# Kernel tuning notes

Hardware: AMD Instinct MI355X
Metric: run time of the kernel (lower is better)

The kernel has to match this reference:

```python
import math
import jax, jax.numpy as jnp
import numpy as np

B, S, E, H = 4, 2048, 1024, 16
HD = E // H  # 64


def setup_inputs() -> dict:
    key = jax.random.key(0)
    ks = jax.random.split(key, 7)
    scale = 1.0 / math.sqrt(E)
    return {
        "x": jax.random.normal(ks[0], (B, S, E), dtype=jnp.float32),
        "Wq": jax.random.normal(ks[1], (H, HD, E), dtype=jnp.float32) * scale,
        "bq": jax.random.normal(ks[2], (H, HD), dtype=jnp.float32) * 0.01,
        "Wk": jax.random.normal(ks[3], (H, HD, E), dtype=jnp.float32) * scale,
        "bk": jax.random.normal(ks[4], (H, HD), dtype=jnp.float32) * 0.01,
        "Wv": jax.random.normal(ks[5], (H, HD, E), dtype=jnp.float32) * scale,
        "bv": jax.random.normal(ks[6], (H, HD), dtype=jnp.float32) * 0.01,
    }


def reference(x, Wq, bq, Wk, bk, Wv, bv):
    b, s, e = x.shape
    h, hd, _ = Wq.shape
    inv_scale = 1.0 / math.sqrt(hd)
    # per-head linear projections (torch Linear: x @ W^T + b), batched over heads
    q = jnp.einsum("bse,hde->bshd", x, Wq) + bq  # [B,S,H,HD]
    k = jnp.einsum("bse,hde->bshd", x, Wk) + bk
    v = jnp.einsum("bse,hde->bshd", x, Wv) + bv
    # causal mask: -inf above diagonal (added before scaling, as in source;
    # -inf * inv_scale is still -inf so math is identical)
    mask = jnp.triu(jnp.full((s, s), -jnp.inf, dtype=x.dtype), k=1)
    scores = (jnp.einsum("bqhd,bkhd->bhqk", q, k) + mask) * inv_scale  # [B,H,S,S]
    attn = jax.nn.softmax(scores, axis=-1)
    out = jnp.einsum("bhqk,bkhd->bqhd", attn, v)  # [B,S,H,HD]
    # concat over heads in head order == reshape with head-major last dims
    return out.reshape(b, s, h * hd)
```

## Files before the change

kernel.cpp:

```cpp
#include <hip/hip_runtime.h>


typedef __bf16 bf16x8 __attribute__((ext_vector_type(8)));
typedef __bf16 bf16x4 __attribute__((ext_vector_type(4)));
typedef float f32x4 __attribute__((ext_vector_type(4)));
typedef unsigned short us8 __attribute__((ext_vector_type(8)));
typedef unsigned short us4 __attribute__((ext_vector_type(4)));

#define Bb 4
#define Ss 2048
#define Ee 1024
#define Hh 16
#define HD 64

#if __has_builtin(__builtin_amdgcn_exp2f)
#define EXP2(x) __builtin_amdgcn_exp2f(x)
#else
#define EXP2(x) exp2f(x)
#endif

__device__ __forceinline__ unsigned short f2bf(float f) {
  union { float f; unsigned u; } v; v.f = f;
  unsigned u = v.u;
  u += 0x7fffu + ((u >> 16) & 1u);
  return (unsigned short)(u >> 16);
}

__device__ __forceinline__ void gl_lds16(const void* g, void* l) {
  __builtin_amdgcn_global_load_lds((const __attribute__((address_space(1))) void*)g,
                                   (__attribute__((address_space(3))) void*)l, 16, 0, 0);
}

#define DSR(d, a, o) asm volatile("ds_read_b128 %0, %1 offset:" #o : "=v"(d) : "v"(a))

__global__ __launch_bounds__(256) void cvt_all(const float* __restrict__ x,
                                               const float* __restrict__ wq,
                                               const float* __restrict__ wk,
                                               const float* __restrict__ wv,
                                               unsigned short* __restrict__ xb,
                                               unsigned short* __restrict__ wb) {
  int i = blockIdx.x * 256 + threadIdx.x;
  const float* src; unsigned short* dst; int idx;
  if (i < 2097152)      { src = x;  dst = xb;                idx = i; }
  else if (i < 2359296) { src = wq; dst = wb;                idx = i - 2097152; }
  else if (i < 2621440) { src = wk; dst = wb + 1048576;      idx = i - 2359296; }
  else                  { src = wv; dst = wb + 2 * 1048576;  idx = i - 2621440; }
  float4 f = ((const float4*)src)[idx];
  us4 o = { f2bf(f.x), f2bf(f.y), f2bf(f.z), f2bf(f.w) };
  ((us4*)dst)[idx] = o;
}

__global__ __launch_bounds__(256, 2) void qkv_gemm(const unsigned short* __restrict__ xb,
                                                   const unsigned short* __restrict__ wb_all,
                                                   const float* __restrict__ bq,
                                                   const float* __restrict__ bk,
                                                   const float* __restrict__ bv,
                                                   unsigned short* __restrict__ qkv) {
  const int z = blockIdx.z;
  const unsigned short* wb = wb_all + (size_t)z * (Ee * Ee);
  const float* bias = (z == 0) ? bq : (z == 1) ? bk : bv;
  unsigned short* outb = qkv + (size_t)z * (Bb * Ss * Ee);
  const float osc = (z == 0) ? 0.180336880f : 1.0f;

  __shared__ unsigned short SMEM[32768];

  const int t = threadIdx.x;
  const int wave = t >> 6, lane = t & 63, quad = lane >> 4, ln = lane & 15;
  const int wr = wave >> 1, wc = wave & 1;
  const int m0 = blockIdx.x * 128, n0 = blockIdx.y * 128;

  const int r32 = t >> 3;
  const int cs = ((t & 7) ^ (r32 & 7)) * 8;
  const int t8 = t * 8;
  const unsigned short* gA0 = xb + (size_t)(m0 + r32) * Ee + cs;
  const unsigned short* gA1 = gA0 + 64 * Ee;
  const unsigned short* gB0 = wb + (size_t)(n0 + r32) * Ee + cs;
  const unsigned short* gB1 = gB0 + 64 * Ee;

  const int swz0 = ((0 * 4 + quad) ^ (ln & 7)) * 16;
  const int swz1 = ((1 * 4 + quad) ^ (ln & 7)) * 16;
  int aA0 = (wr * 32 + ln) * 128 + swz0;
  int aA1 = (wr * 32 + ln) * 128 + swz1;
  int bA0 = 16384 + (wc * 32 + ln) * 128 + swz0;
  int bA1 = 16384 + (wc * 32 + ln) * 128 + swz1;

  f32x4 acc[2][2][2][2] = {};
  bf16x8 af[2][2], bf0[2][2], bf1[2][2];

  gl_lds16(gA0,           &SMEM[t8]);
  gl_lds16(gA0 + 32 * Ee, &SMEM[t8 + 2048]);
  gl_lds16(gB0,           &SMEM[8192 + t8]);
  gl_lds16(gB0 + 32 * Ee, &SMEM[8192 + t8 + 2048]);
  gl_lds16(gB1,           &SMEM[12288 + t8]);
  gl_lds16(gB1 + 32 * Ee, &SMEM[12288 + t8 + 2048]);
  gl_lds16(gA1,           &SMEM[4096 + t8]);
  gl_lds16(gA1 + 32 * Ee, &SMEM[4096 + t8 + 2048]);

#pragma unroll 1
  for (int kt = 0; kt < 15; ++kt) {
    const int sbuf = ((kt & 1) << 14) ^ 16384;
    const int co = (kt + 1) * 64;

    asm volatile("s_waitcnt vmcnt(4)" ::: "memory");
    asm volatile("s_barrier" ::: "memory");
    DSR(af[0][0], aA0, 0);    DSR(af[1][0], aA0, 2048);
    DSR(af[0][1], aA1, 0);    DSR(af[1][1], aA1, 2048);
    DSR(bf0[0][0], bA0, 0);   DSR(bf0[1][0], bA0, 2048);
    DSR(bf0[0][1], bA1, 0);   DSR(bf0[1][1], bA1, 2048);
    gl_lds16(gA0 + co,           &SMEM[sbuf + t8]);
    gl_lds16(gA0 + co + 32 * Ee, &SMEM[sbuf + t8 + 2048]);
    asm volatile("s_barrier" ::: "memory");
    asm volatile("s_waitcnt lgkmcnt(0)" ::: "memory");
    __builtin_amdgcn_sched_barrier(0);
    __builtin_amdgcn_s_setprio(1);
#pragma unroll
    for (int kk = 0; kk < 2; ++kk)
#pragma unroll
      for (int i = 0; i < 2; ++i)
#pragma unroll
        for (int j = 0; j < 2; ++j)
          acc[0][0][i][j] = __builtin_amdgcn_mfma_f32_16x16x32_bf16(af[i][kk], bf0[j][kk], acc[0][0][i][j], 0, 0, 0);
    __builtin_amdgcn_s_setprio(0);
    __builtin_amdgcn_sched_barrier(0);

    asm volatile("s_waitcnt vmcnt(4)" ::: "memory");
    asm volatile("s_barrier" ::: "memory");
    DSR(bf1[0][0], bA0, 8192); DSR(bf1[1][0], bA0, 10240);
    DSR(bf1[0][1], bA1, 8192); DSR(bf1[1][1], bA1, 10240);
    gl_lds16(gB0 + co,           &SMEM[sbuf + 8192 + t8]);
    gl_lds16(gB0 + co + 32 * Ee, &SMEM[sbuf + 8192 + t8 + 2048]);
    asm volatile("s_barrier" ::: "memory");
    asm volatile("s_waitcnt lgkmcnt(0)" ::: "memory");
    __builtin_amdgcn_sched_barrier(0);
    __builtin_amdgcn_s_setprio(1);
#pragma unroll
    for (int kk = 0; kk < 2; ++kk)
#pragma unroll
      for (int i = 0; i < 2; ++i)
#pragma unroll
        for (int j = 0; j < 2; ++j)
          acc[0][1][i][j] = __builtin_amdgcn_mfma_f32_16x16x32_bf16(af[i][kk], bf1[j][kk], acc[0][1][i][j], 0, 0, 0);
    __builtin_amdgcn_s_setprio(0);
    __builtin_amdgcn_sched_barrier(0);

    asm volatile("s_waitcnt vmcnt(4)" ::: "memory");
    asm volatile("s_barrier" ::: "memory");
    DSR(af[0][0], aA0, 8192); DSR(af[1][0], aA0, 10240);
    DSR(af[0][1], aA1, 8192); DSR(af[1][1], aA1, 10240);
    gl_lds16(gB1 + co,           &SMEM[sbuf + 12288 + t8]);
    gl_lds16(gB1 + co + 32 * Ee, &SMEM[sbuf + 12288 + t8 + 2048]);
    asm volatile("s_barrier" ::: "memory");
    asm volatile("s_waitcnt lgkmcnt(0)" ::: "memory");
    __builtin_amdgcn_sched_barrier(0);
    __builtin_amdgcn_s_setprio(1);
#pragma unroll
    for (int kk = 0; kk < 2; ++kk)
#pragma unroll
      for (int i = 0; i < 2; ++i)
#pragma unroll
        for (int j = 0; j < 2; ++j)
          acc[1][0][i][j] = __builtin_amdgcn_mfma_f32_16x16x32_bf16(af[i][kk], bf0[j][kk], acc[1][0][i][j], 0, 0, 0);
    __builtin_amdgcn_s_setprio(0);
    __builtin_amdgcn_sched_barrier(0);

    asm volatile("s_barrier" ::: "memory");
    gl_lds16(gA1 + co,           &SMEM[sbuf + 4096 + t8]);
    gl_lds16(gA1 + co + 32 * Ee, &SMEM[sbuf + 4096 + t8 + 2048]);
    asm volatile("s_barrier" ::: "memory");
    __builtin_amdgcn_sched_barrier(0);
    __builtin_amdgcn_s_setprio(1);
#pragma unroll
    for (int kk = 0; kk < 2; ++kk)
#pragma unroll
      for (int i = 0; i < 2; ++i)
#pragma unroll
        for (int j = 0; j < 2; ++j)
          acc[1][1][i][j] = __builtin_amdgcn_mfma_f32_16x16x32_bf16(af[i][kk], bf1[j][kk], acc[1][1][i][j], 0, 0, 0);
    __builtin_amdgcn_s_setprio(0);
    __builtin_amdgcn_sched_barrier(0);

    aA0 ^= 32768; aA1 ^= 32768; bA0 ^= 32768; bA1 ^= 32768;
  }

  {
    asm volatile("s_waitcnt vmcnt(0)" ::: "memory");
    asm volatile("s_barrier" ::: "memory");
    DSR(af[0][0], aA0, 0);    DSR(af[1][0], aA0, 2048);
    DSR(af[0][1], aA1, 0);    DSR(af[1][1], aA1, 2048);
    DSR(bf0[0][0], bA0, 0);   DSR(bf0[1][0], bA0, 2048);
    DSR(bf0[0][1], bA1, 0);   DSR(bf0[1][1], bA1, 2048);
    DSR(bf1[0][0], bA0, 8192); DSR(bf1[1][0], bA0, 10240);
    DSR(bf1[0][1], bA1, 8192); DSR(bf1[1][1], bA1, 10240);
    asm volatile("s_waitcnt lgkmcnt(0)" ::: "memory");
    __builtin_amdgcn_sched_barrier(0);
#pragma unroll
    for (int kk = 0; kk < 2; ++kk)
#pragma unroll
      for (int i = 0; i < 2; ++i)
#pragma unroll
        for (int j = 0; j < 2; ++j) {
          acc[0][0][i][j] = __builtin_amdgcn_mfma_f32_16x16x32_bf16(af[i][kk], bf0[j][kk], acc[0][0][i][j], 0, 0, 0);
          acc[0][1][i][j] = __builtin_amdgcn_mfma_f32_16x16x32_bf16(af[i][kk], bf1[j][kk], acc[0][1][i][j], 0, 0, 0);
        }
    __builtin_amdgcn_sched_barrier(0);
    DSR(af[0][0], aA0, 8192); DSR(af[1][0], aA0, 10240);
    DSR(af[0][1], aA1, 8192); DSR(af[1][1], aA1, 10240);
    asm volatile("s_waitcnt lgkmcnt(0)" ::: "memory");
    __builtin_amdgcn_sched_barrier(0);
#pragma unroll
    for (int kk = 0; kk < 2; ++kk)
#pragma unroll
      for (int i = 0; i < 2; ++i)
#pragma unroll
        for (int j = 0; j < 2; ++j) {
          acc[1][0][i][j] = __builtin_amdgcn_mfma_f32_16x16x32_bf16(af[i][kk], bf0[j][kk], acc[1][0][i][j], 0, 0, 0);
          acc[1][1][i][j] = __builtin_amdgcn_mfma_f32_16x16x32_bf16(af[i][kk], bf1[j][kk], acc[1][1][i][j], 0, 0, 0);
        }
    __builtin_amdgcn_sched_barrier(0);
  }

  float biasj[2][2];
#pragma unroll
  for (int qb = 0; qb < 2; ++qb)
#pragma unroll
    for (int j = 0; j < 2; ++j)
      biasj[qb][j] = bias[n0 + qb * 64 + wc * 32 + j * 16 + ln];

  if (z != 2) {
#pragma unroll
    for (int qa = 0; qa < 2; ++qa)
#pragma unroll
      for (int qb = 0; qb < 2; ++qb)
#pragma unroll
        for (int i = 0; i < 2; ++i)
#pragma unroll
          for (int j = 0; j < 2; ++j)
#pragma unroll
            for (int r = 0; r < 4; ++r) {
              int m = m0 + qa * 64 + wr * 32 + i * 16 + quad * 4 + r;
              int n = n0 + qb * 64 + wc * 32 + j * 16 + ln;
              int b_ = m >> 11, s = m & 2047;
              int h = n >> 6, d = n & 63;
              outb[(((size_t)b_ * Hh + h) * Ss + s) * HD + d] =
                  f2bf((acc[qa][qb][i][j][r] + biasj[qb][j]) * osc);
            }
  } else {
    __syncthreads();
#pragma unroll
    for (int qa = 0; qa < 2; ++qa)
#pragma unroll
      for (int qb = 0; qb < 2; ++qb)
#pragma unroll
        for (int i = 0; i < 2; ++i)
#pragma unroll
          for (int j = 0; j < 2; ++j)
#pragma unroll
            for (int r = 0; r < 4; ++r) {
              int nc = qb * 64 + wc * 32 + j * 16 + ln;
              int mr = qa * 64 + wr * 32 + i * 16 + quad * 4 + r;
              SMEM[nc * 136 + mr] = f2bf(acc[qa][qb][i][j][r] + biasj[qb][j]);
            }
    __syncthreads();
    int nr = t >> 1, mh = t & 1;
    int n = n0 + nr, h = n >> 6, d = n & 63;
    int b_ = m0 >> 11;
    int s0 = (m0 & 2047) + mh * 64;
#pragma unroll
    for (int q = 0; q < 8; ++q) {
      us8 vdat = *(const us8*)&SMEM[nr * 136 + mh * 64 + q * 8];
      *(us8*)&outb[(((size_t)b_ * Hh + h) * HD + d) * Ss + s0 + q * 8] = vdat;
    }
  }
}

__global__ __launch_bounds__(256, 2) void flash_attn(const unsigned short* __restrict__ qkv,
                                                     float* __restrict__ out) {
  const int id = blockIdx.x;
  const int bh = id & 63;
  const int p = id >> 6;
  const int b_ = bh >> 4, h = bh & 15;

  const unsigned short* qb  = qkv + (size_t)bh * (Ss * HD);
  const unsigned short* kb  = qkv + (size_t)(64 + bh) * (Ss * HD);
  const unsigned short* vtb = qkv + (size_t)(128 + bh) * (Ss * HD);

  __shared__ __bf16 Ks[8192];
  __shared__ __bf16 Vt[8192];
  __shared__ __bf16 Ps[4][16][72];

  const int t = threadIdx.x;
  const int wave = t >> 6, lane = t & 63, quad = lane >> 4, ln = lane & 15;

  const int rk = t >> 3;
  const int ck = ((t & 7) ^ (rk & 7)) * 8;
  const int rv = t >> 4;
  const int cv = ((t & 15) ^ (rv & 7)) * 8;
  const int t8 = t * 8;

  const int qts[2] = { 15 - p, p };
  const int KTB = qts[0] + 1;

  bf16x8 qf[2][2][2];
#pragma unroll
  for (int qt = 0; qt < 2; ++qt)
#pragma unroll
    for (int u = 0; u < 2; ++u)
#pragma unroll
      for (int ks = 0; ks < 2; ++ks)
        qf[qt][u][ks] = *(const bf16x8*)(qb + (size_t)(qts[qt] * 128 + u * 64 + wave * 16 + ln) * HD +
                                         ks * 32 + quad * 8);

  bf16x8 onef;
#pragma unroll
  for (int j = 0; j < 8; ++j) onef[j] = (__bf16)1.0f;

  f32x4 o[2][2][4] = {};
  f32x4 l4[2][2] = {};

#pragma unroll 1
  for (int kt = 0; kt < KTB; ++kt) {
    const unsigned short* kbt = kb + (size_t)kt * (128 * HD);
    const unsigned short* vbt = vtb + kt * 128;
    __syncthreads();
    gl_lds16(kbt + rk * HD + ck,        &Ks[t8]);
    gl_lds16(kbt + (rk + 32) * HD + ck, &Ks[t8 + 2048]);
    gl_lds16(kbt + (rk + 64) * HD + ck, &Ks[t8 + 4096]);
    gl_lds16(kbt + (rk + 96) * HD + ck, &Ks[t8 + 6144]);
    gl_lds16(vbt + rv * Ss + cv,        &Vt[t8]);
    gl_lds16(vbt + (rv + 16) * Ss + cv, &Vt[t8 + 2048]);
    gl_lds16(vbt + (rv + 32) * Ss + cv, &Vt[t8 + 4096]);
    gl_lds16(vbt + (rv + 48) * Ss + cv, &Vt[t8 + 6144]);
    __syncthreads();

#pragma unroll
    for (int h2 = 0; h2 < 2; ++h2) {
      const int kb64 = kt * 2 + h2;
#pragma unroll
      for (int qt = 0; qt < 2; ++qt) {
        const int qtp = qts[qt];
#pragma unroll
        for (int u = 0; u < 2; ++u) {
          const int su = 2 * qtp + u;
          if (kb64 > su) continue;
          const int qrow = qtp * 128 + u * 64 + wave * 16 + ln;

          f32x4 s_acc[4] = {};
#pragma unroll
          for (int g = 0; g < 4; ++g)
#pragma unroll
            for (int ks = 0; ks < 2; ++ks) {
              bf16x8 kf = *(const bf16x8*)&Ks[(h2 * 64 + g * 16 + ln) * 64 +
                                              (((ks * 4 + quad) ^ (ln & 7)) * 8)];
              s_acc[g] = __builtin_amdgcn_mfma_f32_16x16x32_bf16(kf, qf[qt][u][ks], s_acc[g], 0, 0, 0);
            }

          if (kb64 == su) {
            const int k0 = kb64 * 64;
#pragma unroll
            for (int g = 0; g < 4; ++g)
#pragma unroll
              for (int r = 0; r < 4; ++r) {
                int kcol = k0 + g * 16 + quad * 4 + r;
                if (kcol > qrow) s_acc[g][r] = -__builtin_inff();
              }
          }

#pragma unroll
          for (int g = 0; g < 4; ++g) {
            bf16x4 pk = { (__bf16)EXP2(s_acc[g][0]), (__bf16)EXP2(s_acc[g][1]),
                          (__bf16)EXP2(s_acc[g][2]), (__bf16)EXP2(s_acc[g][3]) };
            *(bf16x4*)&Ps[wave][ln][g * 16 + quad * 4] = pk;
          }
          bf16x8 pf[2];
#pragma unroll
          for (int ks = 0; ks < 2; ++ks)
            pf[ks] = *(const bf16x8*)&Ps[wave][ln][ks * 32 + quad * 8];

          l4[qt][u] = __builtin_amdgcn_mfma_f32_16x16x32_bf16(pf[0], onef, l4[qt][u], 0, 0, 0);
          l4[qt][u] = __builtin_amdgcn_mfma_f32_16x16x32_bf16(pf[1], onef, l4[qt][u], 0, 0, 0);

#pragma unroll
          for (int g = 0; g < 4; ++g)
#pragma unroll
            for (int ks = 0; ks < 2; ++ks) {
              bf16x8 vf = *(const bf16x8*)&Vt[(g * 16 + ln) * 128 +
                                              (((h2 * 8 + ks * 4 + quad) ^ (ln & 7)) * 8)];
              o[qt][u][g] = __builtin_amdgcn_mfma_f32_16x16x32_bf16(pf[ks], vf, o[qt][u][g], 0, 0, 0);
            }
        }
      }
    }
  }

#pragma unroll
  for (int qt = 0; qt < 2; ++qt)
#pragma unroll
    for (int u = 0; u < 2; ++u) {
      float linv[4];
#pragma unroll
      for (int r = 0; r < 4; ++r) linv[r] = 1.0f / l4[qt][u][r];
#pragma unroll
      for (int g = 0; g < 4; ++g)
#pragma unroll
        for (int r = 0; r < 4; ++r) {
          int orow = qts[qt] * 128 + u * 64 + wave * 16 + quad * 4 + r;
          out[((size_t)b_ * Ss + orow) * Ee + h * HD + g * 16 + ln] = o[qt][u][g][r] * linv[r];
        }
    }
}

extern "C" void kernel_launch(void* const* d_in, const int* in_sizes, int n_in,
                              void* d_out, int out_size, void* d_ws, size_t ws_size,
                              hipStream_t stream) {
  const float* x  = (const float*)d_in[0];
  const float* Wq = (const float*)d_in[1];
  const float* bq = (const float*)d_in[2];
  const float* Wk = (const float*)d_in[3];
  const float* bk = (const float*)d_in[4];
  const float* Wv = (const float*)d_in[5];
  const float* bv = (const float*)d_in[6];
  float* out = (float*)d_out;

  unsigned short* ws  = (unsigned short*)d_ws;
  unsigned short* xb  = ws;
  unsigned short* wb  = ws + 8388608;
  unsigned short* qkv = ws + 8388608 + 3 * 1048576;

  cvt_all<<<11264, 256, 0, stream>>>(x, Wq, Wk, Wv, xb, wb);
  qkv_gemm<<<dim3(64, 8, 3), 256, 0, stream>>>(xb, wb, bq, bk, bv, qkv);
  flash_attn<<<512, 256, 0, stream>>>(qkv, out);
}
```

Measured before the change: 209.1 us.

## Split flash attention query tiles across eight waves per block

The attention kernel now launches 512 threads per block (8 waves) instead of 256. The two 64-row query halves that each wave used to handle in sequence are now handled by separate waves, and each thread issues half as many K/V tile loads into LDS. This halves per-wave registers and serial work and raises parallelism within the block, in exchange for more waves competing for LDS bandwidth and a larger Ps scratch buffer. The K/V loads and the causal skip logic are remapped to the new wave index.

```diff
diff --git a/kernel.cpp b/kernel.cpp
--- a/kernel.cpp
+++ b/kernel.cpp
@@ -273,7 +273,7 @@
   }
 }
 
-__global__ __launch_bounds__(256, 2) void flash_attn(const unsigned short* __restrict__ qkv,
+__global__ __launch_bounds__(512, 2) void flash_attn(const unsigned short* __restrict__ qkv,
                                                      float* __restrict__ out) {
   const int id = blockIdx.x;
   const int bh = id & 63;
@@ -286,10 +286,11 @@
 
   __shared__ __bf16 Ks[8192];
   __shared__ __bf16 Vt[8192];
-  __shared__ __bf16 Ps[4][16][72];
+  __shared__ __bf16 Ps[8][16][72];
 
   const int t = threadIdx.x;
   const int wave = t >> 6, lane = t & 63, quad = lane >> 4, ln = lane & 15;
+  const int uw = wave >> 2;
 
   const int rk = t >> 3;
   const int ck = ((t & 7) ^ (rk & 7)) * 8;
@@ -300,22 +301,20 @@
   const int qts[2] = { 15 - p, p };
   const int KTB = qts[0] + 1;
 
-  bf16x8 qf[2][2][2];
+  bf16x8 qf[2][2];
 #pragma unroll
   for (int qt = 0; qt < 2; ++qt)
 #pragma unroll
-    for (int u = 0; u < 2; ++u)
-#pragma unroll
-      for (int ks = 0; ks < 2; ++ks)
-        qf[qt][u][ks] = *(const bf16x8*)(qb + (size_t)(qts[qt] * 128 + u * 64 + wave * 16 + ln) * HD +
-                                         ks * 32 + quad * 8);
+    for (int ks = 0; ks < 2; ++ks)
+      qf[qt][ks] = *(const bf16x8*)(qb + (size_t)(qts[qt] * 128 + wave * 16 + ln) * HD +
+                                    ks * 32 + quad * 8);
 
   bf16x8 onef;
 #pragma unroll
   for (int j = 0; j < 8; ++j) onef[j] = (__bf16)1.0f;
 
-  f32x4 o[2][2][4] = {};
-  f32x4 l4[2][2] = {};
+  f32x4 o[2][4] = {};
+  f32x4 l4[2] = {};
 
 #pragma unroll 1
   for (int kt = 0; kt < KTB; ++kt) {
@@ -323,13 +322,9 @@
     const unsigned short* vbt = vtb + kt * 128;
     __syncthreads();
     gl_lds16(kbt + rk * HD + ck,        &Ks[t8]);
-    gl_lds16(kbt + (rk + 32) * HD + ck, &Ks[t8 + 2048]);
     gl_lds16(kbt + (rk + 64) * HD + ck, &Ks[t8 + 4096]);
-    gl_lds16(kbt + (rk + 96) * HD + ck, &Ks[t8 + 6144]);
     gl_lds16(vbt + rv * Ss + cv,        &Vt[t8]);
-    gl_lds16(vbt + (rv + 16) * Ss + cv, &Vt[t8 + 2048]);
     gl_lds16(vbt + (rv + 32) * Ss + cv, &Vt[t8 + 4096]);
-    gl_lds16(vbt + (rv + 48) * Ss + cv, &Vt[t8 + 6144]);
     __syncthreads();
 
 #pragma unroll
@@ -338,75 +333,70 @@
 #pragma unroll
       for (int qt = 0; qt < 2; ++qt) {
         const int qtp = qts[qt];
-#pragma unroll
-        for (int u = 0; u < 2; ++u) {
-          const int su = 2 * qtp + u;
-          if (kb64 > su) continue;
-          const int qrow = qtp * 128 + u * 64 + wave * 16 + ln;
-
-          f32x4 s_acc[4] = {};
+        const int su = 2 * qtp + uw;
+        if (kb64 > su) continue;
+        const int qrow = qtp * 128 + wave * 16 + ln;
+
+        f32x4 s_acc[4] = {};
+#pragma unroll
+        for (int g = 0; g < 4; ++g)
+#pragma unroll
+          for (int ks = 0; ks < 2; ++ks) {
+            bf16x8 kf = *(const bf16x8*)&Ks[(h2 * 64 + g * 16 + ln) * 64 +
+                                            (((ks * 4 + quad) ^ (ln & 7)) * 8)];
+            s_acc[g] = __builtin_amdgcn_mfma_f32_16x16x32_bf16(kf, qf[qt][ks], s_acc[g], 0, 0, 0);
+          }
+
+        if (kb64 == su) {
+          const int k0 = kb64 * 64;
 #pragma unroll
           for (int g = 0; g < 4; ++g)
 #pragma unroll
-            for (int ks = 0; ks < 2; ++ks) {
-              bf16x8 kf = *(const bf16x8*)&Ks[(h2 * 64 + g * 16 + ln) * 64 +
-                                              (((ks * 4 + quad) ^ (ln & 7)) * 8)];
-              s_acc[g] = __builtin_amdgcn_mfma_f32_16x16x32_bf16(kf, qf[qt][u][ks], s_acc[g], 0, 0, 0);
-            }
-
-          if (kb64 == su) {
-            const int k0 = kb64 * 64;
-#pragma unroll
-            for (int g = 0; g < 4; ++g)
-#pragma unroll
-              for (int r = 0; r < 4; ++r) {
-                int kcol = k0 + g * 16 + quad * 4 + r;
-                if (kcol > qrow) s_acc[g][r] = -__builtin_inff();
-              }
-          }
-
-#pragma unroll
-          for (int g = 0; g < 4; ++g) {
-            bf16x4 pk = { (__bf16)EXP2(s_acc[g][0]), (__bf16)EXP2(s_acc[g][1]),
-                          (__bf16)EXP2(s_acc[g][2]), (__bf16)EXP2(s_acc[g][3]) };
-            *(bf16x4*)&Ps[wave][ln][g * 16 + quad * 4] = pk;
-          }
-          bf16x8 pf[2];
-#pragma unroll
-          for (int ks = 0; ks < 2; ++ks)
-            pf[ks] = *(const bf16x8*)&Ps[wave][ln][ks * 32 + quad * 8];
-
-          l4[qt][u] = __builtin_amdgcn_mfma_f32_16x16x32_bf16(pf[0], onef, l4[qt][u], 0, 0, 0);
-          l4[qt][u] = __builtin_amdgcn_mfma_f32_16x16x32_bf16(pf[1], onef, l4[qt][u], 0, 0, 0);
-
-#pragma unroll
-          for (int g = 0; g < 4; ++g)
-#pragma unroll
-            for (int ks = 0; ks < 2; ++ks) {
-              bf16x8 vf = *(const bf16x8*)&Vt[(g * 16 + ln) * 128 +
-                                              (((h2 * 8 + ks * 4 + quad) ^ (ln & 7)) * 8)];
-              o[qt][u][g] = __builtin_amdgcn_mfma_f32_16x16x32_bf16(pf[ks], vf, o[qt][u][g], 0, 0, 0);
+            for (int r = 0; r < 4; ++r) {
+              int kcol = k0 + g * 16 + quad * 4 + r;
+              if (kcol > qrow) s_acc[g][r] = -__builtin_inff();
             }
         }
+
+#pragma unroll
+        for (int g = 0; g < 4; ++g) {
+          bf16x4 pk = { (__bf16)EXP2(s_acc[g][0]), (__bf16)EXP2(s_acc[g][1]),
+                        (__bf16)EXP2(s_acc[g][2]), (__bf16)EXP2(s_acc[g][3]) };
+          *(bf16x4*)&Ps[wave][ln][g * 16 + quad * 4] = pk;
+        }
+        bf16x8 pf[2];
+#pragma unroll
+        for (int ks = 0; ks < 2; ++ks)
+          pf[ks] = *(const bf16x8*)&Ps[wave][ln][ks * 32 + quad * 8];
+
+        l4[qt] = __builtin_amdgcn_mfma_f32_16x16x32_bf16(pf[0], onef, l4[qt], 0, 0, 0);
+        l4[qt] = __builtin_amdgcn_mfma_f32_16x16x32_bf16(pf[1], onef, l4[qt], 0, 0, 0);
+
+#pragma unroll
+        for (int g = 0; g < 4; ++g)
+#pragma unroll
+          for (int ks = 0; ks < 2; ++ks) {
+            bf16x8 vf = *(const bf16x8*)&Vt[(g * 16 + ln) * 128 +
+                                            (((h2 * 8 + ks * 4 + quad) ^ (ln & 7)) * 8)];
+            o[qt][g] = __builtin_amdgcn_mfma_f32_16x16x32_bf16(pf[ks], vf, o[qt][g], 0, 0, 0);
+          }
       }
     }
   }
 
 #pragma unroll
-  for (int qt = 0; qt < 2; ++qt)
-#pragma unroll
-    for (int u = 0; u < 2; ++u) {
-      float linv[4];
-#pragma unroll
-      for (int r = 0; r < 4; ++r) linv[r] = 1.0f / l4[qt][u][r];
-#pragma unroll
-      for (int g = 0; g < 4; ++g)
-#pragma unroll
-        for (int r = 0; r < 4; ++r) {
-          int orow = qts[qt] * 128 + u * 64 + wave * 16 + quad * 4 + r;
-          out[((size_t)b_ * Ss + orow) * Ee + h * HD + g * 16 + ln] = o[qt][u][g][r] * linv[r];
-        }
-    }
+  for (int qt = 0; qt < 2; ++qt) {
+    float linv[4];
+#pragma unroll
+    for (int r = 0; r < 4; ++r) linv[r] = 1.0f / l4[qt][r];
+#pragma unroll
+    for (int g = 0; g < 4; ++g)
+#pragma unroll
+      for (int r = 0; r < 4; ++r) {
+        int orow = qts[qt] * 128 + wave * 16 + quad * 4 + r;
+        out[((size_t)b_ * Ss + orow) * Ee + h * HD + g * 16 + ln] = o[qt][g][r] * linv[r];
+      }
+  }
 }
 
 extern "C" void kernel_launch(void* const* d_in, const int* in_sizes, int n_in,
@@ -428,5 +418,5 @@
 
   cvt_all<<<11264, 256, 0, stream>>>(x, Wq, Wk, Wv, xb, wb);
   qkv_gemm<<<dim3(64, 8, 3), 256, 0, stream>>>(xb, wb, bq, bk, bv, qkv);
-  flash_attn<<<512, 256, 0, stream>>>(qkv, out);
-}
+  flash_attn<<<512, 512, 0, stream>>>(qkv, out);
+}
```

Result: faster. 201.2 us (-3.8%).
